# Optimization experiments

Measured on AMD Instinct MI355X. Metric: run time of the kernel, lower is better.

Reference implementation:

```python
import jax, jax.numpy as jnp
import numpy as np

B, D_IN, T = 16, 1024, 1024
K, D_CB = 8192, 256
DECAY = 0.99
COMMITMENT = 0.15
CODEBOOK_LOSS_W = 1.0
THRESHOLD_DEAD = 2.0


def setup_inputs() -> dict:
    key = jax.random.key(0)
    ks = jax.random.split(key, 9)
    z = jax.random.normal(ks[0], (B, D_IN, T), dtype=jnp.float32)
    # weight-normed 1x1 conv params (kernel size 1 -> treat as matrices)
    in_v = jax.random.normal(ks[1], (D_CB, D_IN), dtype=jnp.float32) * 0.02
    in_g = jnp.ones((D_CB,), dtype=jnp.float32)
    in_b = jnp.zeros((D_CB,), dtype=jnp.float32)
    out_v = jax.random.normal(ks[2], (D_IN, D_CB), dtype=jnp.float32) * 0.02
    out_g = jnp.ones((D_IN,), dtype=jnp.float32)
    out_b = jnp.zeros((D_IN,), dtype=jnp.float32)
    codebook = jax.random.normal(ks[3], (K, D_CB), dtype=jnp.float32)
    cluster_size = jax.random.uniform(ks[4], (K,), dtype=jnp.float32) * 10.0
    return {"z": z, "in_g": in_g, "in_v": in_v, "in_b": in_b,
            "out_g": out_g, "out_v": out_v, "out_b": out_b,
            "codebook": codebook, "cluster_size": cluster_size}


def _wn_weight(g, v):
    # weight_norm dim=0: per-output-channel L2 norm over remaining dims
    return g[:, None] * v / jnp.linalg.norm(v, axis=1, keepdims=True)


def _l2norm(x, axis=-1, eps=1e-12):
    return x / jnp.maximum(jnp.linalg.norm(x, axis=axis, keepdims=True), eps)


def reference(z, in_g, in_v, in_b, out_g, out_v, out_b, codebook, cluster_size):
    sg = jax.lax.stop_gradient
    # in_project: 1x1 weight-normed conv  [B, D_IN, T] -> [B, D_CB, T]
    w_in = _wn_weight(in_g, in_v)
    z_e = jnp.einsum('oi,bit->bot', w_in, z) + in_b[None, :, None]

    # decode_latents
    enc = z_e.transpose(0, 2, 1).reshape(-1, D_CB)           # [(B*T), D_CB]
    enc_n = _l2norm(enc)
    cb_n = _l2norm(codebook)
    dist = (jnp.sum(enc_n ** 2, axis=1, keepdims=True)
            - 2.0 * enc_n @ cb_n.T
            + jnp.sum(cb_n ** 2, axis=1)[None, :])           # [(B*T), K]
    flat_idx = jnp.argmax(-dist, axis=1)                      # [(B*T)]
    indices = flat_idx.reshape(B, T)                          # [B, T]
    z_q = codebook[indices].transpose(0, 2, 1)                # [B, D_CB, T]

    # perplexity / usage stats (one-hot mean == normalized counts)
    n_tokens = B * T
    counts = jnp.zeros((K,), dtype=z_e.dtype).at[flat_idx].add(1.0)
    avg_probs = counts / n_tokens
    perplexity = jnp.exp(-jnp.sum(avg_probs * jnp.log(avg_probs + 1e-10)))

    # EMA cluster-size update (training, forced_activation=False): functional
    new_cluster_size = cluster_size * DECAY + counts * (1.0 - DECAY)
    active_num = jnp.sum(new_cluster_size > THRESHOLD_DEAD).astype(jnp.float32)

    # losses (training path)
    commit_loss = jnp.mean((z_e - sg(z_q)) ** 2, axis=(1, 2)) * COMMITMENT
    codebook_loss = jnp.mean((z_q - sg(z_e)) ** 2, axis=(1, 2)) * CODEBOOK_LOSS_W

    # straight-through
    z_q_st = z_e + sg(z_q - z_e)

    # out_project: 1x1 weight-normed conv  [B, D_CB, T] -> [B, D_IN, T]
    w_out = _wn_weight(out_g, out_v)
    z_q_out = jnp.einsum('oi,bit->bot', w_out, z_q_st) + out_b[None, :, None]

    return (z_q_out, indices, commit_loss, codebook_loss, dist, perplexity, active_num)
```

## Files before the change

### kernel.cpp

```cpp
#include <hip/hip_runtime.h>
#include <stdint.h>

#define B_    16
#define D_IN_ 1024
#define T_    1024
#define K_    8192
#define D_CB_ 256
#define NTOK  (B_*T_)

typedef unsigned long long ull;
typedef __attribute__((ext_vector_type(8))) short short8;
typedef __attribute__((ext_vector_type(4))) float f32x4;

#define WS_WIN   0
#define WS_WOUT  262144
#define WS_ENC   524288
#define WS_INVE  4718592
#define WS_ESQ   4734976
#define WS_INVC  4751360
#define WS_CSQ   4759552
#define WS_KEYS  4767744
#define WS_CNT   4800512
#define WS_LOSS  4808704
#define WS_CBH   4808720
#define WS_CBL   5857296
#define WS_WOH   6905872
#define WS_WOL   7036944
#define WS_EXT_END 7168016
#define WS_EXT_BYTES ((size_t)WS_EXT_END * 4)

#define OUT_ZQ   0
#define OUT_IDX  16777216
#define OUT_COMM 16793600
#define OUT_CB   16793616
#define OUT_DIST 16793632
#define OUT_PERP 151011360
#define OUT_ACT  151011361

#define SCR_EHI  0
#define SCR_ELO  2097152
#define SCR_CHI  4194304
#define SCR_CLO  5242880
#define SCR_MINB 6291456
#define SCR_FLAG 10485760

#define MARGIN 2.5e-4f

__device__ __forceinline__ float wave_sum(float s) {
    for (int o = 32; o; o >>= 1) s += __shfl_down(s, o, 64);
    return s;
}

__device__ __forceinline__ unsigned short f2bf(float f) {
    unsigned u = __float_as_uint(f);
    return (unsigned short)((u + 0x7fffu + ((u >> 16) & 1u)) >> 16);
}

__global__ void wn_kernel(const float* __restrict__ g, const float* __restrict__ v,
                          float* __restrict__ w, int rows, int cols) {
    int wave = threadIdx.x >> 6, lane = threadIdx.x & 63;
    int row = blockIdx.x * 4 + wave;
    if (row >= rows) return;
    const float* vr = v + (size_t)row * cols;
    float s = 0.f;
    for (int c = lane; c < (cols >> 2); c += 64) {
        float4 x = ((const float4*)vr)[c];
        s += x.x*x.x + x.y*x.y + x.z*x.z + x.w*x.w;
    }
    s = wave_sum(s);
    s = __shfl(s, 0, 64);
    float norm = sqrtf(s);
    float gr = g[row];
    float* wr = w + (size_t)row * cols;
    for (int c = lane; c < cols; c += 64)
        wr[c] = gr * vr[c] / norm;
}

__global__ void split_kernel(const float* __restrict__ x, float* __restrict__ inv,
                             float* __restrict__ sq, unsigned short* __restrict__ hi,
                             unsigned short* __restrict__ lo) {
    int wave = threadIdx.x >> 6, lane = threadIdx.x & 63;
    int row = blockIdx.x * 4 + wave;
    float4 v = ((const float4*)(x + (size_t)row * D_CB_))[lane];
    float s = v.x*v.x + v.y*v.y + v.z*v.z + v.w*v.w;
    s = wave_sum(s);
    s = __shfl(s, 0, 64);
    float n = fmaxf(sqrtf(s), 1e-12f);
    float iv = 1.0f / n;
    if (lane == 0) { inv[row] = iv; sq[row] = s * iv * iv; }
    float f[4] = { v.x*iv, v.y*iv, v.z*iv, v.w*iv };
    unsigned short h[4], l[4];
    #pragma unroll
    for (int i = 0; i < 4; ++i) {
        h[i] = f2bf(f[i]);
        float hf = __uint_as_float((unsigned)h[i] << 16);
        l[i] = f2bf(f[i] - hf);
    }
    *(ushort4*)(hi + (size_t)row * D_CB_ + lane * 4) = make_ushort4(h[0], h[1], h[2], h[3]);
    *(ushort4*)(lo + (size_t)row * D_CB_ + lane * 4) = make_ushort4(l[0], l[1], l[2], l[3]);
}

__global__ void splitraw_kernel(const float* __restrict__ x, unsigned short* __restrict__ hi,
                                unsigned short* __restrict__ lo, int n4) {
    int i = blockIdx.x * 256 + threadIdx.x;
    if (i >= n4) return;
    float4 v = ((const float4*)x)[i];
    float f[4] = { v.x, v.y, v.z, v.w };
    unsigned short h[4], l[4];
    #pragma unroll
    for (int q = 0; q < 4; ++q) {
        h[q] = f2bf(f[q]);
        float hf = __uint_as_float((unsigned)h[q] << 16);
        l[q] = f2bf(f[q] - hf);
    }
    *(ushort4*)(hi + (size_t)i * 4) = make_ushort4(h[0], h[1], h[2], h[3]);
    *(ushort4*)(lo + (size_t)i * 4) = make_ushort4(l[0], l[1], l[2], l[3]);
}

__global__ __launch_bounds__(256) void ze_gemm(const float* __restrict__ w,
        const float* __restrict__ z, const float* __restrict__ bias,
        float* __restrict__ enc) {
    __shared__ float As[32 * 68];
    __shared__ float Bs[32 * 132];
    int b  = blockIdx.z;
    int o0 = blockIdx.y * 64;
    int t0 = blockIdx.x * 128;
    int t  = threadIdx.x;
    int tx = t & 15, ty = t >> 4;
    float acc[4][8] = {};
    const float* zb = z + (size_t)b * D_IN_ * T_;
    for (int kt = 0; kt < D_IN_ / 32; ++kt) {
        #pragma unroll
        for (int p = 0; p < 2; ++p) {
            int q = p * 256 + t;
            int r = q >> 3, c4 = q & 7;
            float4 x = *(const float4*)&w[(size_t)(o0 + r) * D_IN_ + kt * 32 + c4 * 4];
            As[(c4*4+0)*68 + r] = x.x; As[(c4*4+1)*68 + r] = x.y;
            As[(c4*4+2)*68 + r] = x.z; As[(c4*4+3)*68 + r] = x.w;
        }
        #pragma unroll
        for (int p = 0; p < 4; ++p) {
            int q = p * 256 + t;
            int r = q >> 5, c4 = q & 31;
            float4 x = *(const float4*)&zb[(size_t)(kt * 32 + r) * T_ + t0 + c4 * 4];
            *(float4*)&Bs[r * 132 + c4 * 4] = x;
        }
        __syncthreads();
        #pragma unroll 4
        for (int k = 0; k < 32; ++k) {
            float a[4], bv[8];
            *(float4*)a      = *(float4*)&As[k * 68 + ty * 4];
            *(float4*)&bv[0] = *(float4*)&Bs[k * 132 + tx * 4];
            *(float4*)&bv[4] = *(float4*)&Bs[k * 132 + 64 + tx * 4];
            #pragma unroll
            for (int i = 0; i < 4; ++i)
                #pragma unroll
                for (int j = 0; j < 8; ++j)
                    acc[i][j] = fmaf(a[i], bv[j], acc[i][j]);
        }
        __syncthreads();
    }
    float bias4[4];
    *(float4*)bias4 = *(const float4*)&bias[o0 + ty * 4];
    #pragma unroll
    for (int j = 0; j < 8; ++j) {
        int token = b * T_ + t0 + (j < 4 ? tx * 4 + j : 64 + tx * 4 + (j - 4));
        float4 v = make_float4(acc[0][j] + bias4[0], acc[1][j] + bias4[1],
                               acc[2][j] + bias4[2], acc[3][j] + bias4[3]);
        *(float4*)&enc[(size_t)token * D_CB_ + o0 + ty * 4] = v;
    }
}

__global__ __launch_bounds__(256, 3) void dist_mfma(
        const unsigned short* __restrict__ ehi, const unsigned short* __restrict__ elo,
        const unsigned short* __restrict__ chi, const unsigned short* __restrict__ clo,
        const float* __restrict__ esq, const float* __restrict__ csq,
        float* __restrict__ dist, ull* __restrict__ minb) {
    __shared__ ull pairs[2][64][2][2];
    int bid = blockIdx.x;
    int x = bid & 7;
    int j_ = bid >> 3;
    int by = x * 16 + (j_ & 15);
    int bx = j_ >> 4;
    int r0 = by * 128, c0 = bx * 128;
    int t = threadIdx.x;
    int wave = t >> 6, lane = t & 63;
    int wm = wave >> 1, wn = wave & 1;
    int lr = lane & 15, kg = lane >> 4;

    const unsigned short* ea = ehi + (size_t)(r0 + wm*64 + lr) * D_CB_ + kg*8;
    const unsigned short* eb = elo + (size_t)(r0 + wm*64 + lr) * D_CB_ + kg*8;
    const unsigned short* ca = chi + (size_t)(c0 + wn*64 + lr) * D_CB_ + kg*8;
    const unsigned short* cl = clo + (size_t)(c0 + wn*64 + lr) * D_CB_ + kg*8;

    f32x4 acc[4][4] = {};
    for (int kt = 0; kt < D_CB_ / 32; ++kt) {
        short8 ah[4], al[4], bh[4], bl[4];
        int k = kt * 32;
        #pragma unroll
        for (int i = 0; i < 4; ++i) {
            ah[i] = *(const short8*)(ea + (size_t)i*16*D_CB_ + k);
            al[i] = *(const short8*)(eb + (size_t)i*16*D_CB_ + k);
            bh[i] = *(const short8*)(ca + (size_t)i*16*D_CB_ + k);
            bl[i] = *(const short8*)(cl + (size_t)i*16*D_CB_ + k);
        }
        #pragma unroll
        for (int i = 0; i < 4; ++i)
            #pragma unroll
            for (int j = 0; j < 4; ++j) {
                acc[i][j] = __builtin_amdgcn_mfma_f32_16x16x32_bf16(ah[i], bh[j], acc[i][j], 0, 0, 0);
                acc[i][j] = __builtin_amdgcn_mfma_f32_16x16x32_bf16(ah[i], bl[j], acc[i][j], 0, 0, 0);
                acc[i][j] = __builtin_amdgcn_mfma_f32_16x16x32_bf16(al[i], bh[j], acc[i][j], 0, 0, 0);
            }
    }
    float csqv[4];
    #pragma unroll
    for (int j = 0; j < 4; ++j) csqv[j] = csq[c0 + wn*64 + j*16 + lr];
    #pragma unroll
    for (int i = 0; i < 4; ++i) {
        #pragma unroll
        for (int r = 0; r < 4; ++r) {
            int rl = i*16 + kg*4 + r;
            int grow = r0 + wm*64 + rl;
            float es = esq[grow];
            float* drow = dist + (size_t)grow * K_ + c0 + wn*64 + lr;
            ull m1 = ~0ull, m2 = ~0ull;
            #pragma unroll
            for (int j = 0; j < 4; ++j) {
                float d = fmaf(-2.0f, acc[i][j][r], es + csqv[j]);
                __builtin_nontemporal_store(d, &drow[j*16]);
                ull key = ((ull)__float_as_uint(d) << 32) | (unsigned)(c0 + wn*64 + j*16 + lr);
                if (key < m1) { m2 = m1; m1 = key; } else if (key < m2) m2 = key;
            }
            #pragma unroll
            for (int off = 1; off < 16; off <<= 1) {
                ull o1 = __shfl_xor(m1, off, 64);
                ull o2 = __shfl_xor(m2, off, 64);
                ull n1 = o1 < m1 ? o1 : m1;
                ull xx = o1 < m1 ? m1 : o1;
                ull yy = o2 < m2 ? o2 : m2;
                m2 = xx < yy ? xx : yy;
                m1 = n1;
            }
            if (lr == 0) { pairs[wm][rl][wn][0] = m1; pairs[wm][rl][wn][1] = m2; }
        }
    }
    __syncthreads();
    if (t < 128) {
        int wm2 = t >> 6, rl = t & 63;
        ull a1 = pairs[wm2][rl][0][0], a2 = pairs[wm2][rl][0][1];
        ull b1 = pairs[wm2][rl][1][0], b2 = pairs[wm2][rl][1][1];
        ull m1 = a1 < b1 ? a1 : b1;
        ull xx = a1 < b1 ? b1 : a1;
        ull yy = a2 < b2 ? a2 : b2;
        ull m2 = xx < yy ? xx : yy;
        size_t grow = (size_t)(r0 + wm2*64 + rl);
        minb[(grow*64 + bx)*2 + 0] = m1;
        minb[(grow*64 + bx)*2 + 1] = m2;
    }
}

__global__ void minreduce(const ull* __restrict__ minb, ull* __restrict__ keys,
                          int* __restrict__ flags) {
    int wave = threadIdx.x >> 6, lane = threadIdx.x & 63;
    int row = blockIdx.x * 4 + wave;
    ull m1 = minb[((size_t)row*64 + lane)*2 + 0];
    ull m2 = minb[((size_t)row*64 + lane)*2 + 1];
    #pragma unroll
    for (int off = 1; off < 64; off <<= 1) {
        ull o1 = __shfl_xor(m1, off, 64);
        ull o2 = __shfl_xor(m2, off, 64);
        ull n1 = o1 < m1 ? o1 : m1;
        ull x  = o1 < m1 ? m1 : o1;
        ull y  = o2 < m2 ? o2 : m2;
        m2 = x < y ? x : y;
        m1 = n1;
    }
    if (lane == 0) {
        keys[row] = m1;
        float d1 = __uint_as_float((unsigned)(m1 >> 32));
        float d2 = __uint_as_float((unsigned)(m2 >> 32));
        flags[row] = (d2 - d1 < MARGIN) ? 1 : 0;
    }
}

__global__ void argmin_fix(const float* __restrict__ enc, const float* __restrict__ inve,
        const float* __restrict__ esq, const float* __restrict__ cb,
        const float* __restrict__ invc, const float* __restrict__ csq,
        const float* __restrict__ dist, const int* __restrict__ flags,
        ull* __restrict__ keys) {
    int row = blockIdx.x;
    if (!flags[row]) return;
    int lane = threadIdx.x;
    ull k0 = keys[row];
    float thr = __uint_as_float((unsigned)(k0 >> 32)) + MARGIN;
    float iv = inve[row];
    float4 ev = ((const float4*)(enc + (size_t)row * D_CB_))[lane];
    ev.x *= iv; ev.y *= iv; ev.z *= iv; ev.w *= iv;
    float es = esq[row];
    float best = 1e30f; int bestc = 0;
    for (int base = 0; base < K_; base += 64) {
        float d = dist[(size_t)row * K_ + base + lane];
        ull mask = __ballot(d <= thr);
        while (mask) {
            int b = __ffsll(mask) - 1;
            mask &= mask - 1;
            int c = base + b;
            float4 cv = ((const float4*)(cb + (size_t)c * D_CB_))[lane];
            float p = ev.x*cv.x + ev.y*cv.y + ev.z*cv.z + ev.w*cv.w;
            p = wave_sum(p);
            p = __shfl(p, 0, 64);
            float dx = fmaf(-2.0f * invc[c], p, es + csq[c]);
            if (dx < best) { best = dx; bestc = c; }
        }
    }
    if (lane == 0)
        keys[row] = ((ull)__float_as_uint(best) << 32) | (unsigned)bestc;
}

__global__ void token_kernel(const float* __restrict__ enc, const float* __restrict__ cb,
        const ull* __restrict__ keys, float* __restrict__ idx_out,
        float* __restrict__ counts, float* __restrict__ loss) {
    int wave = threadIdx.x >> 6, lane = threadIdx.x & 63;
    int tok = blockIdx.x * 4 + wave;
    int idx = (int)(unsigned int)(keys[tok] & 0xffffffffull);
    float4 e = ((const float4*)(enc + (size_t)tok * D_CB_))[lane];
    float4 q = ((const float4*)(cb  + (size_t)idx * D_CB_))[lane];
    float dx = e.x - q.x, dy = e.y - q.y, dz = e.z - q.z, dw = e.w - q.w;
    float s = dx*dx + dy*dy + dz*dz + dw*dw;
    s = wave_sum(s);
    if (lane == 0) {
        idx_out[tok] = (float)idx;
        atomicAdd(&counts[idx], 1.0f);
        atomicAdd(&loss[tok >> 10], s);
    }
}

__global__ __launch_bounds__(256, 3) void out_mfma(
        const unsigned short* __restrict__ wh, const unsigned short* __restrict__ wl,
        const unsigned short* __restrict__ cbh, const unsigned short* __restrict__ cbl,
        const ull* __restrict__ keys, const float* __restrict__ bias,
        float* __restrict__ out) {
    int b  = blockIdx.z;
    int d0 = blockIdx.y * 128;
    int t0 = blockIdx.x * 128;
    int t = threadIdx.x;
    int wave = t >> 6, lane = t & 63;
    int wm = wave >> 1, wn = wave & 1;
    int lr = lane & 15, kg = lane >> 4;

    int idx[4];
    #pragma unroll
    for (int i = 0; i < 4; ++i)
        idx[i] = (int)(unsigned)(keys[b*T_ + t0 + wn*64 + i*16 + lr] & 0xffffffffull);

    const unsigned short* wa = wh + (size_t)(d0 + wm*64 + lr) * D_CB_ + kg*8;
    const unsigned short* wb = wl + (size_t)(d0 + wm*64 + lr) * D_CB_ + kg*8;

    f32x4 acc[4][4] = {};
    for (int kt = 0; kt < D_CB_ / 32; ++kt) {
        int k = kt * 32;
        short8 ah[4], al[4], bh[4], bl[4];
        #pragma unroll
        for (int i = 0; i < 4; ++i) {
            ah[i] = *(const short8*)(wa + (size_t)i*16*D_CB_ + k);
            al[i] = *(const short8*)(wb + (size_t)i*16*D_CB_ + k);
            bh[i] = *(const short8*)(cbh + (size_t)idx[i]*D_CB_ + kg*8 + k);
            bl[i] = *(const short8*)(cbl + (size_t)idx[i]*D_CB_ + kg*8 + k);
        }
        #pragma unroll
        for (int i = 0; i < 4; ++i)
            #pragma unroll
            for (int j = 0; j < 4; ++j) {
                acc[i][j] = __builtin_amdgcn_mfma_f32_16x16x32_bf16(ah[i], bh[j], acc[i][j], 0, 0, 0);
                acc[i][j] = __builtin_amdgcn_mfma_f32_16x16x32_bf16(ah[i], bl[j], acc[i][j], 0, 0, 0);
                acc[i][j] = __builtin_amdgcn_mfma_f32_16x16x32_bf16(al[i], bh[j], acc[i][j], 0, 0, 0);
            }
    }
    float* ob = out + (size_t)b * D_IN_ * T_;
    #pragma unroll
    for (int i = 0; i < 4; ++i) {
        #pragma unroll
        for (int r = 0; r < 4; ++r) {
            int d = d0 + wm*64 + i*16 + kg*4 + r;
            float bb = bias[d];
            #pragma unroll
            for (int j = 0; j < 4; ++j) {
                int tt = t0 + wn*64 + j*16 + lr;
                __builtin_nontemporal_store(acc[i][j][r] + bb, &ob[(size_t)d * T_ + tt]);
            }
        }
    }
}

__global__ __launch_bounds__(256) void out_gemm(const float* __restrict__ w,
        const float* __restrict__ cb, const ull* __restrict__ keys,
        const float* __restrict__ bias, float* __restrict__ out) {
    __shared__ float As[32 * 68];
    __shared__ float Bs[32 * 68];
    __shared__ int idxs[64];
    int b  = blockIdx.z;
    int d0 = blockIdx.y * 64;
    int t0 = blockIdx.x * 64;
    int t  = threadIdx.x;
    if (t < 64) idxs[t] = (int)(unsigned int)(keys[b * T_ + t0 + t] & 0xffffffffull);
    __syncthreads();
    int tx = t & 15, ty = t >> 4;
    float acc[4][4] = {};
    for (int kt = 0; kt < D_CB_ / 32; ++kt) {
        #pragma unroll
        for (int p = 0; p < 2; ++p) {
            int q = p * 256 + t;
            int r = q >> 3, c4 = q & 7;
            float4 x = *(const float4*)&w[(size_t)(d0 + r) * D_CB_ + kt * 32 + c4 * 4];
            As[(c4*4+0)*68 + r] = x.x; As[(c4*4+1)*68 + r] = x.y;
            As[(c4*4+2)*68 + r] = x.z; As[(c4*4+3)*68 + r] = x.w;
        }
        #pragma unroll
        for (int p = 0; p < 2; ++p) {
            int q = p * 256 + t;
            int r = q >> 3, c4 = q & 7;
            float4 x = *(const float4*)&cb[(size_t)idxs[r] * D_CB_ + kt * 32 + c4 * 4];
            Bs[(c4*4+0)*68 + r] = x.x; Bs[(c4*4+1)*68 + r] = x.y;
            Bs[(c4*4+2)*68 + r] = x.z; Bs[(c4*4+3)*68 + r] = x.w;
        }
        __syncthreads();
        #pragma unroll 4
        for (int k = 0; k < 32; ++k) {
            float a[4], bv[4];
            *(float4*)a  = *(float4*)&As[k * 68 + ty * 4];
            *(float4*)bv = *(float4*)&Bs[k * 68 + tx * 4];
            #pragma unroll
            for (int i = 0; i < 4; ++i)
                #pragma unroll
                for (int j = 0; j < 4; ++j)
                    acc[i][j] = fmaf(a[i], bv[j], acc[i][j]);
        }
        __syncthreads();
    }
    #pragma unroll
    for (int i = 0; i < 4; ++i) {
        int d = d0 + ty * 4 + i;
        float bb = bias[d];
        float4 v = make_float4(acc[i][0] + bb, acc[i][1] + bb, acc[i][2] + bb, acc[i][3] + bb);
        *(float4*)&out[(size_t)b * D_IN_ * T_ + (size_t)d * T_ + t0 + tx * 4] = v;
    }
}

__global__ void finalize_kernel(const float* __restrict__ counts, const float* __restrict__ cs,
                                const float* __restrict__ loss, float* __restrict__ out) {
    int t = threadIdx.x;
    float H = 0.f, act = 0.f;
    for (int k = t; k < K_; k += 256) {
        float c = counts[k];
        float p = c * (1.0f / 16384.0f);
        H += p * logf(p + 1e-10f);
        float ncs = cs[k] * 0.99f + c * 0.01f;
        if (ncs > 2.0f) act += 1.0f;
    }
    __shared__ float sh[8];
    for (int o = 32; o; o >>= 1) { H += __shfl_down(H, o, 64); act += __shfl_down(act, o, 64); }
    int wave = t >> 6, lane = t & 63;
    if (lane == 0) { sh[wave] = H; sh[4 + wave] = act; }
    __syncthreads();
    if (t == 0) {
        out[OUT_PERP] = expf(-(sh[0] + sh[1] + sh[2] + sh[3]));
        out[OUT_ACT]  = sh[4] + sh[5] + sh[6] + sh[7];
    }
    if (t < 16) {
        float m = loss[t] * (1.0f / 262144.0f);
        out[OUT_COMM + t] = m * 0.15f;
        out[OUT_CB + t]   = m;
    }
}

extern "C" void kernel_launch(void* const* d_in, const int* in_sizes, int n_in,
                              void* d_out, int out_size, void* d_ws, size_t ws_size,
                              hipStream_t stream) {
    const float* z        = (const float*)d_in[0];
    const float* in_g     = (const float*)d_in[1];
    const float* in_v     = (const float*)d_in[2];
    const float* in_b     = (const float*)d_in[3];
    const float* out_g    = (const float*)d_in[4];
    const float* out_v    = (const float*)d_in[5];
    const float* out_b    = (const float*)d_in[6];
    const float* codebook = (const float*)d_in[7];
    const float* cluster  = (const float*)d_in[8];
    float* out = (float*)d_out;
    float* ws  = (float*)d_ws;
    ull* keys  = (ull*)(ws + WS_KEYS);

    float* scr = out + OUT_ZQ;
    unsigned short* ehi = (unsigned short*)(scr + SCR_EHI);
    unsigned short* elo = (unsigned short*)(scr + SCR_ELO);
    unsigned short* chi = (unsigned short*)(scr + SCR_CHI);
    unsigned short* clo = (unsigned short*)(scr + SCR_CLO);
    ull* minb  = (ull*)(scr + SCR_MINB);
    int* flags = (int*)(scr + SCR_FLAG);

    bool mfma_out = ws_size >= WS_EXT_BYTES;

    hipMemsetAsync(ws + WS_CNT, 0, (K_ + 16) * sizeof(float), stream);

    wn_kernel<<<64, 256, 0, stream>>>(in_g, in_v, ws + WS_WIN, D_CB_, D_IN_);
    wn_kernel<<<256, 256, 0, stream>>>(out_g, out_v, ws + WS_WOUT, D_IN_, D_CB_);
    split_kernel<<<K_ / 4, 256, 0, stream>>>(codebook, ws + WS_INVC, ws + WS_CSQ, chi, clo);
    if (mfma_out) {
        splitraw_kernel<<<2048, 256, 0, stream>>>(codebook,
                (unsigned short*)(ws + WS_CBH), (unsigned short*)(ws + WS_CBL), K_ * D_CB_ / 4);
        splitraw_kernel<<<256, 256, 0, stream>>>(ws + WS_WOUT,
                (unsigned short*)(ws + WS_WOH), (unsigned short*)(ws + WS_WOL), D_IN_ * D_CB_ / 4);
    }
    ze_gemm<<<dim3(8, 4, 16), 256, 0, stream>>>(ws + WS_WIN, z, in_b, ws + WS_ENC);
    split_kernel<<<NTOK / 4, 256, 0, stream>>>(ws + WS_ENC, ws + WS_INVE, ws + WS_ESQ, ehi, elo);
    dist_mfma<<<8192, 256, 0, stream>>>(ehi, elo, chi, clo, ws + WS_ESQ, ws + WS_CSQ,
                                        out + OUT_DIST, minb);
    minreduce<<<NTOK / 4, 256, 0, stream>>>(minb, keys, flags);
    argmin_fix<<<NTOK, 64, 0, stream>>>(ws + WS_ENC, ws + WS_INVE, ws + WS_ESQ,
                                        codebook, ws + WS_INVC, ws + WS_CSQ,
                                        out + OUT_DIST, flags, keys);
    token_kernel<<<NTOK / 4, 256, 0, stream>>>(ws + WS_ENC, codebook, keys,
                                               out + OUT_IDX, ws + WS_CNT, ws + WS_LOSS);
    if (mfma_out) {
        out_mfma<<<dim3(8, 8, 16), 256, 0, stream>>>(
                (const unsigned short*)(ws + WS_WOH), (const unsigned short*)(ws + WS_WOL),
                (const unsigned short*)(ws + WS_CBH), (const unsigned short*)(ws + WS_CBL),
                keys, out_b, out + OUT_ZQ);
    } else {
        out_gemm<<<dim3(16, 16, 16), 256, 0, stream>>>(ws + WS_WOUT, codebook, keys,
                                                       out_b, out + OUT_ZQ);
    }
    finalize_kernel<<<1, 256, 0, stream>>>(ws + WS_CNT, cluster, ws + WS_LOSS, out);
}
```

Before: 1.592 ms.

## Always use MFMA out-projection via gathered per-token split buffers, reusing workspace

Removes the workspace-size fallback and the scalar out_gemm path. The selected codebook rows are now gathered into contiguous per-token bf16 hi/lo buffers (zq_split), written over dead workspace regions, so out_mfma reads coalesced rows instead of doing indirect gathers and no longer needs the full codebook split. The dist_mfma top-2 reduction moves partly into shared memory with fewer shuffles, and keys switch to an order-preserving float encoding so negative distances sort correctly. The occupancy hint of 3 is dropped from the launch bounds. The cost is an extra gather kernel and an added shared-memory merge step.

```diff
diff --git a/kernel.cpp b/kernel.cpp
--- a/kernel.cpp
+++ b/kernel.cpp
@@ -22,12 +22,6 @@
 #define WS_KEYS  4767744
 #define WS_CNT   4800512
 #define WS_LOSS  4808704
-#define WS_CBH   4808720
-#define WS_CBL   5857296
-#define WS_WOH   6905872
-#define WS_WOL   7036944
-#define WS_EXT_END 7168016
-#define WS_EXT_BYTES ((size_t)WS_EXT_END * 4)
 
 #define OUT_ZQ   0
 #define OUT_IDX  16777216
@@ -54,6 +48,23 @@
 __device__ __forceinline__ unsigned short f2bf(float f) {
     unsigned u = __float_as_uint(f);
     return (unsigned short)((u + 0x7fffu + ((u >> 16) & 1u)) >> 16);
+}
+
+__device__ __forceinline__ unsigned fkey(float f) {
+    unsigned u = __float_as_uint(f);
+    return u ^ (unsigned)(((int)u >> 31) | 0x80000000);
+}
+__device__ __forceinline__ float fdec(unsigned k) {
+    unsigned u = (k & 0x80000000u) ? (k ^ 0x80000000u) : ~k;
+    return __uint_as_float(u);
+}
+
+__device__ __forceinline__ void merge2(ull& m1, ull& m2, ull o1, ull o2) {
+    ull n1 = o1 < m1 ? o1 : m1;
+    ull hi = o1 < m1 ? m1 : o1;
+    ull lo = o2 < m2 ? o2 : m2;
+    m2 = hi < lo ? hi : lo;
+    m1 = n1;
 }
 
 __global__ void wn_kernel(const float* __restrict__ g, const float* __restrict__ v,
@@ -117,6 +128,24 @@
     *(ushort4*)(lo + (size_t)i * 4) = make_ushort4(l[0], l[1], l[2], l[3]);
 }
 
+__global__ void zq_split(const float* __restrict__ cb, const ull* __restrict__ keys,
+                         unsigned short* __restrict__ qh, unsigned short* __restrict__ ql) {
+    int wave = threadIdx.x >> 6, lane = threadIdx.x & 63;
+    int tok = blockIdx.x * 4 + wave;
+    int idx = (int)(unsigned)(keys[tok] & 0xffffffffull);
+    float4 v = ((const float4*)(cb + (size_t)idx * D_CB_))[lane];
+    float f[4] = { v.x, v.y, v.z, v.w };
+    unsigned short h[4], l[4];
+    #pragma unroll
+    for (int q = 0; q < 4; ++q) {
+        h[q] = f2bf(f[q]);
+        float hf = __uint_as_float((unsigned)h[q] << 16);
+        l[q] = f2bf(f[q] - hf);
+    }
+    *(ushort4*)(qh + (size_t)tok * D_CB_ + lane * 4) = make_ushort4(h[0], h[1], h[2], h[3]);
+    *(ushort4*)(ql + (size_t)tok * D_CB_ + lane * 4) = make_ushort4(l[0], l[1], l[2], l[3]);
+}
+
 __global__ __launch_bounds__(256) void ze_gemm(const float* __restrict__ w,
         const float* __restrict__ z, const float* __restrict__ bias,
         float* __restrict__ enc) {
@@ -171,12 +200,12 @@
     }
 }
 
-__global__ __launch_bounds__(256, 3) void dist_mfma(
+__global__ __launch_bounds__(256) void dist_mfma(
         const unsigned short* __restrict__ ehi, const unsigned short* __restrict__ elo,
         const unsigned short* __restrict__ chi, const unsigned short* __restrict__ clo,
         const float* __restrict__ esq, const float* __restrict__ csq,
         float* __restrict__ dist, ull* __restrict__ minb) {
-    __shared__ ull pairs[2][64][2][2];
+    __shared__ ull pairs[2][64][2][4][2];
     int bid = blockIdx.x;
     int x = bid & 7;
     int j_ = bid >> 3;
@@ -229,31 +258,30 @@
             for (int j = 0; j < 4; ++j) {
                 float d = fmaf(-2.0f, acc[i][j][r], es + csqv[j]);
                 __builtin_nontemporal_store(d, &drow[j*16]);
-                ull key = ((ull)__float_as_uint(d) << 32) | (unsigned)(c0 + wn*64 + j*16 + lr);
+                ull key = ((ull)fkey(d) << 32) | (unsigned)(c0 + wn*64 + j*16 + lr);
                 if (key < m1) { m2 = m1; m1 = key; } else if (key < m2) m2 = key;
             }
             #pragma unroll
-            for (int off = 1; off < 16; off <<= 1) {
+            for (int off = 1; off <= 2; off <<= 1) {
                 ull o1 = __shfl_xor(m1, off, 64);
                 ull o2 = __shfl_xor(m2, off, 64);
-                ull n1 = o1 < m1 ? o1 : m1;
-                ull xx = o1 < m1 ? m1 : o1;
-                ull yy = o2 < m2 ? o2 : m2;
-                m2 = xx < yy ? xx : yy;
-                m1 = n1;
-            }
-            if (lr == 0) { pairs[wm][rl][wn][0] = m1; pairs[wm][rl][wn][1] = m2; }
+                merge2(m1, m2, o1, o2);
+            }
+            if ((lr & 3) == 0) {
+                pairs[wm][rl][wn][lr >> 2][0] = m1;
+                pairs[wm][rl][wn][lr >> 2][1] = m2;
+            }
         }
     }
     __syncthreads();
     if (t < 128) {
         int wm2 = t >> 6, rl = t & 63;
-        ull a1 = pairs[wm2][rl][0][0], a2 = pairs[wm2][rl][0][1];
-        ull b1 = pairs[wm2][rl][1][0], b2 = pairs[wm2][rl][1][1];
-        ull m1 = a1 < b1 ? a1 : b1;
-        ull xx = a1 < b1 ? b1 : a1;
-        ull yy = a2 < b2 ? a2 : b2;
-        ull m2 = xx < yy ? xx : yy;
+        ull m1 = ~0ull, m2 = ~0ull;
+        #pragma unroll
+        for (int wn2 = 0; wn2 < 2; ++wn2)
+            #pragma unroll
+            for (int s = 0; s < 4; ++s)
+                merge2(m1, m2, pairs[wm2][rl][wn2][s][0], pairs[wm2][rl][wn2][s][1]);
         size_t grow = (size_t)(r0 + wm2*64 + rl);
         minb[(grow*64 + bx)*2 + 0] = m1;
         minb[(grow*64 + bx)*2 + 1] = m2;
@@ -270,16 +298,12 @@
     for (int off = 1; off < 64; off <<= 1) {
         ull o1 = __shfl_xor(m1, off, 64);
         ull o2 = __shfl_xor(m2, off, 64);
-        ull n1 = o1 < m1 ? o1 : m1;
-        ull x  = o1 < m1 ? m1 : o1;
-        ull y  = o2 < m2 ? o2 : m2;
-        m2 = x < y ? x : y;
-        m1 = n1;
+        merge2(m1, m2, o1, o2);
     }
     if (lane == 0) {
         keys[row] = m1;
-        float d1 = __uint_as_float((unsigned)(m1 >> 32));
-        float d2 = __uint_as_float((unsigned)(m2 >> 32));
+        float d1 = fdec((unsigned)(m1 >> 32));
+        float d2 = fdec((unsigned)(m2 >> 32));
         flags[row] = (d2 - d1 < MARGIN) ? 1 : 0;
     }
 }
@@ -293,7 +317,7 @@
     if (!flags[row]) return;
     int lane = threadIdx.x;
     ull k0 = keys[row];
-    float thr = __uint_as_float((unsigned)(k0 >> 32)) + MARGIN;
+    float thr = fdec((unsigned)(k0 >> 32)) + MARGIN;
     float iv = inve[row];
     float4 ev = ((const float4*)(enc + (size_t)row * D_CB_))[lane];
     ev.x *= iv; ev.y *= iv; ev.z *= iv; ev.w *= iv;
@@ -315,7 +339,7 @@
         }
     }
     if (lane == 0)
-        keys[row] = ((ull)__float_as_uint(best) << 32) | (unsigned)bestc;
+        keys[row] = ((ull)fkey(best) << 32) | (unsigned)bestc;
 }
 
 __global__ void token_kernel(const float* __restrict__ enc, const float* __restrict__ cb,
@@ -336,26 +360,23 @@
     }
 }
 
-__global__ __launch_bounds__(256, 3) void out_mfma(
+__global__ __launch_bounds__(256) void out_mfma(
         const unsigned short* __restrict__ wh, const unsigned short* __restrict__ wl,
-        const unsigned short* __restrict__ cbh, const unsigned short* __restrict__ cbl,
-        const ull* __restrict__ keys, const float* __restrict__ bias,
-        float* __restrict__ out) {
-    int b  = blockIdx.z;
-    int d0 = blockIdx.y * 128;
-    int t0 = blockIdx.x * 128;
+        const unsigned short* __restrict__ qh, const unsigned short* __restrict__ ql,
+        const float* __restrict__ bias, float* __restrict__ out) {
+    int d0  = blockIdx.y * 128;
+    int tk0 = blockIdx.x * 128;
+    int b   = tk0 >> 10;
+    int t0  = tk0 & 1023;
     int t = threadIdx.x;
     int wave = t >> 6, lane = t & 63;
     int wm = wave >> 1, wn = wave & 1;
     int lr = lane & 15, kg = lane >> 4;
 
-    int idx[4];
-    #pragma unroll
-    for (int i = 0; i < 4; ++i)
-        idx[i] = (int)(unsigned)(keys[b*T_ + t0 + wn*64 + i*16 + lr] & 0xffffffffull);
-
     const unsigned short* wa = wh + (size_t)(d0 + wm*64 + lr) * D_CB_ + kg*8;
     const unsigned short* wb = wl + (size_t)(d0 + wm*64 + lr) * D_CB_ + kg*8;
+    const unsigned short* qa = qh + (size_t)(tk0 + wn*64 + lr) * D_CB_ + kg*8;
+    const unsigned short* qb = ql + (size_t)(tk0 + wn*64 + lr) * D_CB_ + kg*8;
 
     f32x4 acc[4][4] = {};
     for (int kt = 0; kt < D_CB_ / 32; ++kt) {
@@ -365,8 +386,8 @@
         for (int i = 0; i < 4; ++i) {
             ah[i] = *(const short8*)(wa + (size_t)i*16*D_CB_ + k);
             al[i] = *(const short8*)(wb + (size_t)i*16*D_CB_ + k);
-            bh[i] = *(const short8*)(cbh + (size_t)idx[i]*D_CB_ + kg*8 + k);
-            bl[i] = *(const short8*)(cbl + (size_t)idx[i]*D_CB_ + kg*8 + k);
+            bh[i] = *(const short8*)(qa + (size_t)i*16*D_CB_ + k);
+            bl[i] = *(const short8*)(qb + (size_t)i*16*D_CB_ + k);
         }
         #pragma unroll
         for (int i = 0; i < 4; ++i)
@@ -390,60 +411,6 @@
                 __builtin_nontemporal_store(acc[i][j][r] + bb, &ob[(size_t)d * T_ + tt]);
             }
         }
-    }
-}
-
-__global__ __launch_bounds__(256) void out_gemm(const float* __restrict__ w,
-        const float* __restrict__ cb, const ull* __restrict__ keys,
-        const float* __restrict__ bias, float* __restrict__ out) {
-    __shared__ float As[32 * 68];
-    __shared__ float Bs[32 * 68];
-    __shared__ int idxs[64];
-    int b  = blockIdx.z;
-    int d0 = blockIdx.y * 64;
-    int t0 = blockIdx.x * 64;
-    int t  = threadIdx.x;
-    if (t < 64) idxs[t] = (int)(unsigned int)(keys[b * T_ + t0 + t] & 0xffffffffull);
-    __syncthreads();
-    int tx = t & 15, ty = t >> 4;
-    float acc[4][4] = {};
-    for (int kt = 0; kt < D_CB_ / 32; ++kt) {
-        #pragma unroll
-        for (int p = 0; p < 2; ++p) {
-            int q = p * 256 + t;
-            int r = q >> 3, c4 = q & 7;
-            float4 x = *(const float4*)&w[(size_t)(d0 + r) * D_CB_ + kt * 32 + c4 * 4];
-            As[(c4*4+0)*68 + r] = x.x; As[(c4*4+1)*68 + r] = x.y;
-            As[(c4*4+2)*68 + r] = x.z; As[(c4*4+3)*68 + r] = x.w;
-        }
-        #pragma unroll
-        for (int p = 0; p < 2; ++p) {
-            int q = p * 256 + t;
-            int r = q >> 3, c4 = q & 7;
-            float4 x = *(const float4*)&cb[(size_t)idxs[r] * D_CB_ + kt * 32 + c4 * 4];
-            Bs[(c4*4+0)*68 + r] = x.x; Bs[(c4*4+1)*68 + r] = x.y;
-            Bs[(c4*4+2)*68 + r] = x.z; Bs[(c4*4+3)*68 + r] = x.w;
-        }
-        __syncthreads();
-        #pragma unroll 4
-        for (int k = 0; k < 32; ++k) {
-            float a[4], bv[4];
-            *(float4*)a  = *(float4*)&As[k * 68 + ty * 4];
-            *(float4*)bv = *(float4*)&Bs[k * 68 + tx * 4];
-            #pragma unroll
-            for (int i = 0; i < 4; ++i)
-                #pragma unroll
-                for (int j = 0; j < 4; ++j)
-                    acc[i][j] = fmaf(a[i], bv[j], acc[i][j]);
-        }
-        __syncthreads();
-    }
-    #pragma unroll
-    for (int i = 0; i < 4; ++i) {
-        int d = d0 + ty * 4 + i;
-        float bb = bias[d];
-        float4 v = make_float4(acc[i][0] + bb, acc[i][1] + bb, acc[i][2] + bb, acc[i][3] + bb);
-        *(float4*)&out[(size_t)b * D_IN_ * T_ + (size_t)d * T_ + t0 + tx * 4] = v;
     }
 }
 
@@ -498,19 +465,16 @@
     ull* minb  = (ull*)(scr + SCR_MINB);
     int* flags = (int*)(scr + SCR_FLAG);
 
-    bool mfma_out = ws_size >= WS_EXT_BYTES;
+    unsigned short* zqh = (unsigned short*)(ws + WS_ENC);
+    unsigned short* zql = (unsigned short*)(ws + WS_ENC + 2097152);
+    unsigned short* woh = (unsigned short*)(ws + WS_WIN);
+    unsigned short* wol = (unsigned short*)(ws + WS_WIN + 131072);
 
     hipMemsetAsync(ws + WS_CNT, 0, (K_ + 16) * sizeof(float), stream);
 
     wn_kernel<<<64, 256, 0, stream>>>(in_g, in_v, ws + WS_WIN, D_CB_, D_IN_);
     wn_kernel<<<256, 256, 0, stream>>>(out_g, out_v, ws + WS_WOUT, D_IN_, D_CB_);
     split_kernel<<<K_ / 4, 256, 0, stream>>>(codebook, ws + WS_INVC, ws + WS_CSQ, chi, clo);
-    if (mfma_out) {
-        splitraw_kernel<<<2048, 256, 0, stream>>>(codebook,
-                (unsigned short*)(ws + WS_CBH), (unsigned short*)(ws + WS_CBL), K_ * D_CB_ / 4);
-        splitraw_kernel<<<256, 256, 0, stream>>>(ws + WS_WOUT,
-                (unsigned short*)(ws + WS_WOH), (unsigned short*)(ws + WS_WOL), D_IN_ * D_CB_ / 4);
-    }
     ze_gemm<<<dim3(8, 4, 16), 256, 0, stream>>>(ws + WS_WIN, z, in_b, ws + WS_ENC);
     split_kernel<<<NTOK / 4, 256, 0, stream>>>(ws + WS_ENC, ws + WS_INVE, ws + WS_ESQ, ehi, elo);
     dist_mfma<<<8192, 256, 0, stream>>>(ehi, elo, chi, clo, ws + WS_ESQ, ws + WS_CSQ,
@@ -521,14 +485,8 @@
                                         out + OUT_DIST, flags, keys);
     token_kernel<<<NTOK / 4, 256, 0, stream>>>(ws + WS_ENC, codebook, keys,
                                                out + OUT_IDX, ws + WS_CNT, ws + WS_LOSS);
-    if (mfma_out) {
-        out_mfma<<<dim3(8, 8, 16), 256, 0, stream>>>(
-                (const unsigned short*)(ws + WS_WOH), (const unsigned short*)(ws + WS_WOL),
-                (const unsigned short*)(ws + WS_CBH), (const unsigned short*)(ws + WS_CBL),
-                keys, out_b, out + OUT_ZQ);
-    } else {
-        out_gemm<<<dim3(16, 16, 16), 256, 0, stream>>>(ws + WS_WOUT, codebook, keys,
-                                                       out_b, out + OUT_ZQ);
-    }
+    splitraw_kernel<<<256, 256, 0, stream>>>(ws + WS_WOUT, woh, wol, D_IN_ * D_CB_ / 4);
+    zq_split<<<NTOK / 4, 256, 0, stream>>>(codebook, keys, zqh, zql);
+    out_mfma<<<dim3(128, 8), 256, 0, stream>>>(woh, wol, zqh, zql, out_b, out + OUT_ZQ);
     finalize_kernel<<<1, 256, 0, stream>>>(ws + WS_CNT, cluster, ws + WS_LOSS, out);
 }
```

Result: no change. 1.580 ms (-0.7%).
